# Optimization experiments

Hardware: AMD Instinct MI355X
Metric: run time of the kernel (lower is better)

## Reference

```python
import jax, jax.numpy as jnp
import numpy as np

N_NODES = 20000
N_EDGES = 640000
F_IN = 128
HID = 128


def setup_inputs() -> dict:
    key = jax.random.key(0)
    ks = jax.random.split(key, 12)
    d = {}
    d["x"] = jax.random.normal(ks[0], (N_NODES, F_IN), dtype=jnp.float32)
    d["edge_index"] = jax.random.randint(ks[1], (2, N_EDGES), 0, N_NODES, dtype=jnp.int64)
    d["edge_weight"] = jax.random.uniform(ks[2], (N_EDGES,), dtype=jnp.float32)
    d["h"] = jax.random.normal(ks[3], (N_NODES, HID), dtype=jnp.float32)
    s1 = 1.0 / np.sqrt(F_IN)
    s2 = 1.0 / np.sqrt(HID)
    s3 = 1.0 / np.sqrt(2 * HID)
    d["W1"] = jax.random.uniform(ks[4], (F_IN, HID), jnp.float32, -s1, s1)
    d["b1"] = jnp.zeros((HID,), jnp.float32)
    d["W2"] = jax.random.uniform(ks[5], (HID, HID), jnp.float32, -s2, s2)
    d["b2"] = jnp.zeros((HID,), jnp.float32)
    d["Wu"] = jax.random.uniform(ks[6], (2 * HID, HID), jnp.float32, -s3, s3)
    d["bu"] = jax.random.uniform(ks[7], (HID,), jnp.float32, -s3, s3)
    d["Wr"] = jax.random.uniform(ks[8], (2 * HID, HID), jnp.float32, -s3, s3)
    d["br"] = jax.random.uniform(ks[9], (HID,), jnp.float32, -s3, s3)
    d["Wc"] = jax.random.uniform(ks[10], (2 * HID, HID), jnp.float32, -s3, s3)
    d["bc"] = jax.random.uniform(ks[11], (HID,), jnp.float32, -s3, s3)
    return d


def _gcn_layer(x, W, b, src, dst, norm, n):
    # GCNConv: transform then normalized scatter-add aggregation
    xw = x @ W                                    # [N, out]
    agg = jax.ops.segment_sum(xw[src] * norm[:, None], dst, num_segments=n)
    return agg + b


def reference(x, edge_index, edge_weight, h, W1, b1, W2, b2, Wu, bu, Wr, br, Wc, bc):
    n = x.shape[0]
    loops = jnp.arange(n, dtype=edge_index.dtype)
    src = jnp.concatenate([edge_index[0], loops])
    dst = jnp.concatenate([edge_index[1], loops])
    ew = jnp.concatenate([edge_weight, jnp.ones((n,), edge_weight.dtype)])
    # symmetric GCN normalization with self-loops
    deg = jax.ops.segment_sum(ew, dst, num_segments=n)
    dinv = jnp.where(deg > 0, jax.lax.rsqrt(deg), 0.0)
    norm = dinv[src] * ew * dinv[dst]             # [E+N]
    # 2-layer GCN: in->hid (ReLU) -> hid->hid
    h1 = jax.nn.relu(_gcn_layer(x, W1, b1, src, dst, norm, n))
    g = _gcn_layer(h1, W2, b2, src, dst, norm, n)
    xg = jax.nn.sigmoid(g)                        # [N, HID]
    # GRU-style gating
    xh = jnp.concatenate([xg, h], axis=-1)        # [N, 2*HID]
    u = jax.nn.sigmoid(xh @ Wu + bu)
    r = jax.nn.sigmoid(xh @ Wr + br)
    c = jnp.tanh(jnp.concatenate([xg, r * h], axis=-1) @ Wc + bc)
    return u * h + (1.0 - u) * c
```

## Files before the change

kernel.cpp:

```cpp
#include <hip/hip_runtime.h>
#include <math.h>

#define N_NODES 20000
#define N_EDGES 640000
#define HID 128
#define NPAD 20224
#define NBLK 79
#define NSHARD 8

typedef __attribute__((ext_vector_type(8))) short bf16x8;
typedef __attribute__((ext_vector_type(4))) float f32x4;

#define FIX_SCALE 274877906944.0
#define FIX_MASK ((1ull << 48) - 1)

__device__ inline short f2bf(float f) {
    unsigned u = __builtin_bit_cast(unsigned, f);
    u += 0x7fffu + ((u >> 16) & 1u);
    return (short)(u >> 16);
}
__device__ inline float bf2f(short s) {
    unsigned u = ((unsigned)(unsigned short)s) << 16;
    return __builtin_bit_cast(float, u);
}
__device__ inline float4 unpack_bf4(uint2 v) {
    float4 f;
    f.x = __builtin_bit_cast(float, v.x << 16);
    f.y = __builtin_bit_cast(float, v.x & 0xffff0000u);
    f.z = __builtin_bit_cast(float, v.y << 16);
    f.w = __builtin_bit_cast(float, v.y & 0xffff0000u);
    return f;
}
__device__ inline uint2 pack_bf4(float4 f) {
    uint2 v;
    v.x = (unsigned)(unsigned short)f2bf(f.x) | ((unsigned)(unsigned short)f2bf(f.y) << 16);
    v.y = (unsigned)(unsigned short)f2bf(f.z) | ((unsigned)(unsigned short)f2bf(f.w) << 16);
    return v;
}
__device__ inline bf16x8 cvt8(float4 a0, float4 a1) {
    bf16x8 v;
    v[0] = f2bf(a0.x); v[1] = f2bf(a0.y); v[2] = f2bf(a0.z); v[3] = f2bf(a0.w);
    v[4] = f2bf(a1.x); v[5] = f2bf(a1.y); v[6] = f2bf(a1.z); v[7] = f2bf(a1.w);
    return v;
}

__global__ __launch_bounds__(256) void k_init(unsigned long long* packed) {
    int i = blockIdx.x * 256 + threadIdx.x;
    if (i < NSHARD * NPAD) packed[i] = 0ull;
}

__global__ __launch_bounds__(256) void k_hist(unsigned long long* packed, int* __restrict__ rank,
                                              const int* __restrict__ dst,
                                              const float* __restrict__ ew) {
    int e = blockIdx.x * 256 + threadIdx.x;
    int shard = blockIdx.x & (NSHARD - 1);
    if (e < N_EDGES) {
        int d = dst[e];
        unsigned long long add = (1ull << 48) | (unsigned long long)((double)ew[e] * FIX_SCALE);
        unsigned long long old = atomicAdd(&packed[shard * NPAD + d], add);
        rank[e] = (int)(old >> 48);
    }
}

__global__ __launch_bounds__(256) void k_scan_part(const unsigned long long* __restrict__ packed,
                                                   int* __restrict__ tot, int* __restrict__ bsum) {
    __shared__ int red[256];
    int tid = threadIdx.x;
    int i = blockIdx.x * 256 + tid;
    int t = 0;
    if (i < N_NODES) {
#pragma unroll
        for (int s = 0; s < NSHARD; s++) t += (int)(packed[s * NPAD + i] >> 48);
        tot[i] = t;
    }
    red[tid] = t;
    __syncthreads();
    for (int off = 128; off > 0; off >>= 1) {
        if (tid < off) red[tid] += red[tid + off];
        __syncthreads();
    }
    if (tid == 0) bsum[blockIdx.x] = red[0];
}

__global__ __launch_bounds__(256) void k_scan_final(const unsigned long long* __restrict__ packed,
                                                    const int* __restrict__ tot,
                                                    const int* __restrict__ bsum,
                                                    int* __restrict__ rp, int* __restrict__ sb,
                                                    float* __restrict__ dinv) {
    __shared__ int smem[256];
    __shared__ int red[256];
    int tid = threadIdx.x;
    red[tid] = (tid < blockIdx.x) ? bsum[tid] : 0;
    int i = blockIdx.x * 256 + tid;
    int t = (i < N_NODES) ? tot[i] : 0;
    smem[tid] = t;
    __syncthreads();
    for (int off = 128; off > 0; off >>= 1) {
        if (tid < off) red[tid] += red[tid + off];
        __syncthreads();
    }
    for (int off = 1; off < 256; off <<= 1) {
        int x = (tid >= off) ? smem[tid - off] : 0;
        __syncthreads();
        smem[tid] += x;
        __syncthreads();
    }
    if (i < N_NODES) {
        int excl = smem[tid] - t + red[0];
        rp[i] = excl;
        if (i == N_NODES - 1) rp[N_NODES] = excl + t;
        int acc = excl;
        double deg = 1.0;
#pragma unroll
        for (int s = 0; s < NSHARD; s++) {
            unsigned long long p = packed[s * NPAD + i];
            sb[s * NPAD + i] = acc;
            acc += (int)(p >> 48);
            deg += (double)(p & FIX_MASK) * (1.0 / FIX_SCALE);
        }
        dinv[i] = rsqrtf((float)deg);
    }
}

__global__ __launch_bounds__(256) void k_fill(const int* __restrict__ src,
                                              const int* __restrict__ dst,
                                              const float* __restrict__ ew,
                                              const float* __restrict__ dinv,
                                              const int* __restrict__ sb,
                                              const int* __restrict__ rank,
                                              int2* __restrict__ csr) {
    int e = blockIdx.x * 256 + threadIdx.x;
    int shard = blockIdx.x & (NSHARD - 1);
    if (e < N_EDGES) {
        int s = src[e], d = dst[e];
        int slot = sb[shard * NPAD + d] + rank[e];
        float w = dinv[s] * ew[e] * dinv[d];
        csr[slot] = make_int2(s, __builtin_bit_cast(int, w));
    }
}

__global__ __launch_bounds__(256) void k_wcvt(const float* __restrict__ W1, const float* __restrict__ W2,
                                              const float* __restrict__ Wu, const float* __restrict__ Wr,
                                              const float* __restrict__ Wc,
                                              short* WT1, short* WT2, short* WTu, short* WTr, short* WTc) {
    int i = blockIdx.x * 256 + threadIdx.x;
    if (i < 32768) {
        const float* W = (i < 16384) ? W1 : W2;
        short* T = (i < 16384) ? WT1 : WT2;
        int j = i & 16383;
        int n = j >> 7, k = j & 127;
        T[n * 128 + k] = f2bf(W[k * 128 + n]);
    } else {
        int j = i - 32768;
        const float* W = Wu; short* T = WTu;
        if (j >= 65536)      { W = Wc; T = WTc; j -= 65536; }
        else if (j >= 32768) { W = Wr; T = WTr; j -= 32768; }
        int n = j >> 8, k = j & 255;
        T[n * 256 + k] = f2bf(W[k * 128 + n]);
    }
}

__global__ __launch_bounds__(256) void k_gemm_mfma(const float* __restrict__ Af,
                                                   const short* __restrict__ Ab,
                                                   const short* __restrict__ WT,
                                                   short* __restrict__ Cb) {
    __shared__ short As[16 * 136];
    int tid = threadIdx.x;
    int r0 = blockIdx.x * 16;
    {
        int row = tid >> 4;
        int col0 = (tid & 15) * 8;
        bf16x8 v;
        if (Af) {
            const float* p = Af + (size_t)(r0 + row) * HID + col0;
            v = cvt8(*(const float4*)p, *(const float4*)(p + 4));
        } else {
            v = *(const bf16x8*)(Ab + (size_t)(r0 + row) * HID + col0);
        }
        *(bf16x8*)(&As[row * 136 + col0]) = v;
    }
    __syncthreads();
    int wave = tid >> 6, lane = tid & 63;
    int m = lane & 15, quad = lane >> 4;
    f32x4 acc[2];
    acc[0] = (f32x4){0.f, 0.f, 0.f, 0.f};
    acc[1] = acc[0];
#pragma unroll
    for (int ks = 0; ks < 4; ks++) {
        int k0 = ks * 32 + quad * 8;
        bf16x8 a = *(const bf16x8*)(&As[m * 136 + k0]);
#pragma unroll
        for (int j = 0; j < 2; j++) {
            int n = (wave * 2 + j) * 16 + m;
            bf16x8 b = *(const bf16x8*)(WT + n * 128 + k0);
            acc[j] = __builtin_amdgcn_mfma_f32_16x16x32_bf16(a, b, acc[j], 0, 0, 0);
        }
    }
#pragma unroll
    for (int j = 0; j < 2; j++) {
        int col = (wave * 2 + j) * 16 + m;
#pragma unroll
        for (int rg = 0; rg < 4; rg++) {
            int grow = r0 + quad * 4 + rg;
            Cb[(size_t)grow * HID + col] = f2bf(acc[j][rg]);
        }
    }
}

__global__ __launch_bounds__(256) void k_aggregate(const short* __restrict__ xw,
                                                   short* __restrict__ outb,
                                                   const int* __restrict__ rp,
                                                   const int2* __restrict__ csr,
                                                   const float* __restrict__ dinv,
                                                   const float* __restrict__ bias,
                                                   int act) {
    int node = blockIdx.x * 4 + (threadIdx.x >> 6);
    int lane = threadIdx.x & 63;
    int half = lane >> 5;
    int l = lane & 31;
    float4 acc = {0.f, 0.f, 0.f, 0.f};
    if (half == 0) {
        float dv = dinv[node];
        float dv2 = dv * dv;
        float4 v = unpack_bf4(((const uint2*)(xw + (size_t)node * HID))[l]);
        acc.x = v.x * dv2; acc.y = v.y * dv2; acc.z = v.z * dv2; acc.w = v.w * dv2;
    }
    int j = rp[node], end = rp[node + 1];
    for (; j + 15 < end; j += 16) {
        int2 e[8];
#pragma unroll
        for (int i = 0; i < 8; i++) e[i] = csr[j + 2 * i + half];
        float4 v[8];
#pragma unroll
        for (int i = 0; i < 8; i++) v[i] = unpack_bf4(((const uint2*)(xw + (size_t)e[i].x * HID))[l]);
#pragma unroll
        for (int i = 0; i < 8; i++) {
            float w = __builtin_bit_cast(float, e[i].y);
            acc.x += v[i].x * w; acc.y += v[i].y * w; acc.z += v[i].z * w; acc.w += v[i].w * w;
        }
    }
    for (; j + 7 < end; j += 8) {
        int2 e[4];
#pragma unroll
        for (int i = 0; i < 4; i++) e[i] = csr[j + 2 * i + half];
        float4 v[4];
#pragma unroll
        for (int i = 0; i < 4; i++) v[i] = unpack_bf4(((const uint2*)(xw + (size_t)e[i].x * HID))[l]);
#pragma unroll
        for (int i = 0; i < 4; i++) {
            float w = __builtin_bit_cast(float, e[i].y);
            acc.x += v[i].x * w; acc.y += v[i].y * w; acc.z += v[i].z * w; acc.w += v[i].w * w;
        }
    }
    for (; j + 1 < end; j += 2) {
        int2 e0 = csr[j + half];
        float4 v0 = unpack_bf4(((const uint2*)(xw + (size_t)e0.x * HID))[l]);
        float w0 = __builtin_bit_cast(float, e0.y);
        acc.x += v0.x * w0; acc.y += v0.y * w0; acc.z += v0.z * w0; acc.w += v0.w * w0;
    }
    if (j < end && half == 0) {
        int2 e0 = csr[j];
        float4 v0 = unpack_bf4(((const uint2*)(xw + (size_t)e0.x * HID))[l]);
        float w0 = __builtin_bit_cast(float, e0.y);
        acc.x += v0.x * w0; acc.y += v0.y * w0; acc.z += v0.z * w0; acc.w += v0.w * w0;
    }
    acc.x += __shfl_xor(acc.x, 32);
    acc.y += __shfl_xor(acc.y, 32);
    acc.z += __shfl_xor(acc.z, 32);
    acc.w += __shfl_xor(acc.w, 32);
    if (half == 0) {
        float4 b = ((const float4*)bias)[l];
        acc.x += b.x; acc.y += b.y; acc.z += b.z; acc.w += b.w;
        if (act == 0) {
            acc.x = fmaxf(acc.x, 0.f); acc.y = fmaxf(acc.y, 0.f);
            acc.z = fmaxf(acc.z, 0.f); acc.w = fmaxf(acc.w, 0.f);
        } else {
            acc.x = 1.f / (1.f + __expf(-acc.x)); acc.y = 1.f / (1.f + __expf(-acc.y));
            acc.z = 1.f / (1.f + __expf(-acc.z)); acc.w = 1.f / (1.f + __expf(-acc.w));
        }
        ((uint2*)(outb + (size_t)node * HID))[l] = pack_bf4(acc);
    }
}

__global__ __launch_bounds__(256) void k_gate(const short* __restrict__ xgb,
                                              const float* __restrict__ hf,
                                              const short* __restrict__ WTu, const short* __restrict__ WTr,
                                              const short* __restrict__ WTc,
                                              const float* __restrict__ pbu, const float* __restrict__ pbr,
                                              const float* __restrict__ pbc,
                                              float* __restrict__ out) {
    __shared__ short Xs[16 * 264];
    int tid = threadIdx.x;
    int r0 = blockIdx.x * 16;
#pragma unroll
    for (int i = 0; i < 2; i++) {
        int c = tid + i * 256;
        int row = c >> 5;
        int col0 = (c & 31) * 8;
        int grow = r0 + row;
        bf16x8 v;
        if (col0 < 128) {
            v = *(const bf16x8*)(xgb + (size_t)grow * HID + col0);
        } else {
            const float* p = hf + (size_t)grow * HID + (col0 - 128);
            v = cvt8(*(const float4*)p, *(const float4*)(p + 4));
        }
        *(bf16x8*)(&Xs[row * 264 + col0]) = v;
    }
    __syncthreads();
    int wave = tid >> 6, lane = tid & 63;
    int m = lane & 15, quad = lane >> 4;
    f32x4 au[2], ar[2];
    au[0] = (f32x4){0.f, 0.f, 0.f, 0.f};
    au[1] = au[0]; ar[0] = au[0]; ar[1] = au[0];
#pragma unroll
    for (int ks = 0; ks < 8; ks++) {
        int k0 = ks * 32 + quad * 8;
        bf16x8 a = *(const bf16x8*)(&Xs[m * 264 + k0]);
#pragma unroll
        for (int j = 0; j < 2; j++) {
            int n = (wave * 2 + j) * 16 + m;
            bf16x8 bu_f = *(const bf16x8*)(WTu + n * 256 + k0);
            au[j] = __builtin_amdgcn_mfma_f32_16x16x32_bf16(a, bu_f, au[j], 0, 0, 0);
            bf16x8 br_f = *(const bf16x8*)(WTr + n * 256 + k0);
            ar[j] = __builtin_amdgcn_mfma_f32_16x16x32_bf16(a, br_f, ar[j], 0, 0, 0);
        }
    }
    __syncthreads();
#pragma unroll
    for (int j = 0; j < 2; j++) {
        int col = (wave * 2 + j) * 16 + m;
        float brv = pbr[col];
#pragma unroll
        for (int rg = 0; rg < 4; rg++) {
            int trow = quad * 4 + rg;
            float rv = 1.f / (1.f + __expf(-(ar[j][rg] + brv)));
            float hv = bf2f(Xs[trow * 264 + 128 + col]);
            Xs[trow * 264 + 128 + col] = f2bf(rv * hv);
        }
    }
    __syncthreads();
    f32x4 ac[2];
    ac[0] = (f32x4){0.f, 0.f, 0.f, 0.f};
    ac[1] = ac[0];
#pragma unroll
    for (int ks = 0; ks < 8; ks++) {
        int k0 = ks * 32 + quad * 8;
        bf16x8 a = *(const bf16x8*)(&Xs[m * 264 + k0]);
#pragma unroll
        for (int j = 0; j < 2; j++) {
            int n = (wave * 2 + j) * 16 + m;
            bf16x8 bc_f = *(const bf16x8*)(WTc + n * 256 + k0);
            ac[j] = __builtin_amdgcn_mfma_f32_16x16x32_bf16(a, bc_f, ac[j], 0, 0, 0);
        }
    }
#pragma unroll
    for (int j = 0; j < 2; j++) {
        int col = (wave * 2 + j) * 16 + m;
        float buv = pbu[col], bcv = pbc[col];
#pragma unroll
        for (int rg = 0; rg < 4; rg++) {
            int grow = r0 + quad * 4 + rg;
            float uv = 1.f / (1.f + __expf(-(au[j][rg] + buv)));
            float cv = tanhf(ac[j][rg] + bcv);
            float hv = hf[(size_t)grow * HID + col];
            out[(size_t)grow * HID + col] = uv * hv + (1.f - uv) * cv;
        }
    }
}

extern "C" void kernel_launch(void* const* d_in, const int* in_sizes, int n_in,
                              void* d_out, int out_size, void* d_ws, size_t ws_size,
                              hipStream_t stream) {
    const float* x  = (const float*)d_in[0];
    const int*   ei = (const int*)d_in[1];
    const float* ew = (const float*)d_in[2];
    const float* h  = (const float*)d_in[3];
    const float* W1 = (const float*)d_in[4];
    const float* b1 = (const float*)d_in[5];
    const float* W2 = (const float*)d_in[6];
    const float* b2 = (const float*)d_in[7];
    const float* Wu = (const float*)d_in[8];
    const float* bu = (const float*)d_in[9];
    const float* Wr = (const float*)d_in[10];
    const float* br = (const float*)d_in[11];
    const float* Wc = (const float*)d_in[12];
    const float* bc = (const float*)d_in[13];
    const int* src = ei;
    const int* dst = ei + N_EDGES;
    float* out = (float*)d_out;

    const size_t NH = (size_t)N_NODES * HID;
    float* ws = (float*)d_ws;
    float* dinv = ws;
    int*   rp   = (int*)(ws + NPAD);
    unsigned long long* packed = (unsigned long long*)(ws + 2 * NPAD);
    int*   sb   = (int*)(ws + 18 * NPAD);
    int*   tot  = (int*)(ws + 26 * NPAD);
    int*   bsum = (int*)(ws + 27 * NPAD);
    int*   rank = (int*)(ws + 27 * NPAD + 128);
    int2*  csr  = (int2*)(ws + 27 * NPAD + 128 + N_EDGES);
    short* xw  = (short*)(ws + 27 * NPAD + 128 + 3 * N_EDGES);
    short* h1b = xw + NH;
    short* xgb = h1b + NH;
    short* WT1 = xgb + NH;
    short* WT2 = WT1 + 16384;
    short* WTu = WT2 + 16384;
    short* WTr = WTu + 32768;
    short* WTc = WTr + 32768;

    k_init<<<(NSHARD * NPAD + 255) / 256, 256, 0, stream>>>(packed);
    k_hist<<<N_EDGES / 256, 256, 0, stream>>>(packed, rank, dst, ew);
    k_scan_part<<<NBLK, 256, 0, stream>>>(packed, tot, bsum);
    k_scan_final<<<NBLK, 256, 0, stream>>>(packed, tot, bsum, rp, sb, dinv);
    k_fill<<<N_EDGES / 256, 256, 0, stream>>>(src, dst, ew, dinv, sb, rank, csr);

    k_wcvt<<<512, 256, 0, stream>>>(W1, W2, Wu, Wr, Wc, WT1, WT2, WTu, WTr, WTc);

    k_gemm_mfma<<<N_NODES / 16, 256, 0, stream>>>(x, nullptr, WT1, xw);
    k_aggregate<<<N_NODES / 4, 256, 0, stream>>>(xw, h1b, rp, csr, dinv, b1, 0);
    k_gemm_mfma<<<N_NODES / 16, 256, 0, stream>>>(nullptr, h1b, WT2, xw);
    k_aggregate<<<N_NODES / 4, 256, 0, stream>>>(xw, xgb, rp, csr, dinv, b2, 1);
    k_gate<<<N_NODES / 16, 256, 0, stream>>>(xgb, h, WTu, WTr, WTc, bu, br, bc, out);
}
```

Measured before the change: 252.1 us.

## Fuse GCN aggregation with following GEMMs and merge setup kernels

Merges the weight conversion with the histogram-buffer zeroing, and runs the edge histogram alongside the first-layer GEMM in a single launch. Each aggregation now writes its result straight into shared memory, where the next GEMM (W2, or the gating GEMMs) consumes it. This removes launches and the round-trips of the h1 and xg intermediates through global memory. The cost is that aggregation is now done by 16-row blocks, with each wave handling 4 nodes in sequence, which gives less parallelism and may leave blocks imbalanced by node degree.

```diff
diff --git a/kernel.cpp b/kernel.cpp
--- a/kernel.cpp
+++ b/kernel.cpp
@@ -44,21 +44,142 @@
     return v;
 }
 
-__global__ __launch_bounds__(256) void k_init(unsigned long long* packed) {
-    int i = blockIdx.x * 256 + threadIdx.x;
-    if (i < NSHARD * NPAD) packed[i] = 0ull;
-}
-
-__global__ __launch_bounds__(256) void k_hist(unsigned long long* packed, int* __restrict__ rank,
-                                              const int* __restrict__ dst,
-                                              const float* __restrict__ ew) {
-    int e = blockIdx.x * 256 + threadIdx.x;
-    int shard = blockIdx.x & (NSHARD - 1);
-    if (e < N_EDGES) {
+__device__ inline float4 agg_node(int node, int half, int l,
+                                  const short* __restrict__ xw,
+                                  const int* __restrict__ rp,
+                                  const int2* __restrict__ csr,
+                                  const float* __restrict__ dinv) {
+    float4 acc = {0.f, 0.f, 0.f, 0.f};
+    if (half == 0) {
+        float dv = dinv[node];
+        float dv2 = dv * dv;
+        float4 v = unpack_bf4(((const uint2*)(xw + (size_t)node * HID))[l]);
+        acc.x = v.x * dv2; acc.y = v.y * dv2; acc.z = v.z * dv2; acc.w = v.w * dv2;
+    }
+    int j = rp[node], end = rp[node + 1];
+    for (; j + 15 < end; j += 16) {
+        int2 e[8];
+#pragma unroll
+        for (int i = 0; i < 8; i++) e[i] = csr[j + 2 * i + half];
+        float4 v[8];
+#pragma unroll
+        for (int i = 0; i < 8; i++) v[i] = unpack_bf4(((const uint2*)(xw + (size_t)e[i].x * HID))[l]);
+#pragma unroll
+        for (int i = 0; i < 8; i++) {
+            float w = __builtin_bit_cast(float, e[i].y);
+            acc.x += v[i].x * w; acc.y += v[i].y * w; acc.z += v[i].z * w; acc.w += v[i].w * w;
+        }
+    }
+    for (; j + 7 < end; j += 8) {
+        int2 e[4];
+#pragma unroll
+        for (int i = 0; i < 4; i++) e[i] = csr[j + 2 * i + half];
+        float4 v[4];
+#pragma unroll
+        for (int i = 0; i < 4; i++) v[i] = unpack_bf4(((const uint2*)(xw + (size_t)e[i].x * HID))[l]);
+#pragma unroll
+        for (int i = 0; i < 4; i++) {
+            float w = __builtin_bit_cast(float, e[i].y);
+            acc.x += v[i].x * w; acc.y += v[i].y * w; acc.z += v[i].z * w; acc.w += v[i].w * w;
+        }
+    }
+    for (; j + 1 < end; j += 2) {
+        int2 e0 = csr[j + half];
+        float4 v0 = unpack_bf4(((const uint2*)(xw + (size_t)e0.x * HID))[l]);
+        float w0 = __builtin_bit_cast(float, e0.y);
+        acc.x += v0.x * w0; acc.y += v0.y * w0; acc.z += v0.z * w0; acc.w += v0.w * w0;
+    }
+    if (j < end && half == 0) {
+        int2 e0 = csr[j];
+        float4 v0 = unpack_bf4(((const uint2*)(xw + (size_t)e0.x * HID))[l]);
+        float w0 = __builtin_bit_cast(float, e0.y);
+        acc.x += v0.x * w0; acc.y += v0.y * w0; acc.z += v0.z * w0; acc.w += v0.w * w0;
+    }
+    acc.x += __shfl_xor(acc.x, 32);
+    acc.y += __shfl_xor(acc.y, 32);
+    acc.z += __shfl_xor(acc.z, 32);
+    acc.w += __shfl_xor(acc.w, 32);
+    return acc;
+}
+
+__global__ __launch_bounds__(256) void k_prep(const float* __restrict__ W1, const float* __restrict__ W2,
+                                              const float* __restrict__ Wu, const float* __restrict__ Wr,
+                                              const float* __restrict__ Wc,
+                                              short* WT1, short* WT2, short* WTu, short* WTr, short* WTc,
+                                              unsigned long long* packed) {
+    int b = blockIdx.x;
+    int tid = threadIdx.x;
+    if (b < 512) {
+        int i = b * 256 + tid;
+        if (i < 32768) {
+            const float* W = (i < 16384) ? W1 : W2;
+            short* T = (i < 16384) ? WT1 : WT2;
+            int j = i & 16383;
+            int n = j >> 7, k = j & 127;
+            T[n * 128 + k] = f2bf(W[k * 128 + n]);
+        } else {
+            int j = i - 32768;
+            const float* W = Wu; short* T = WTu;
+            if (j >= 65536)      { W = Wc; T = WTc; j -= 65536; }
+            else if (j >= 32768) { W = Wr; T = WTr; j -= 32768; }
+            int n = j >> 8, k = j & 255;
+            T[n * 256 + k] = f2bf(W[k * 128 + n]);
+        }
+    } else {
+        int i = (b - 512) * 256 + tid;
+        if (i < NSHARD * NPAD) packed[i] = 0ull;
+    }
+}
+
+__global__ __launch_bounds__(256) void k_hist_gemm(unsigned long long* packed, int* __restrict__ rank,
+                                                   const int* __restrict__ dst,
+                                                   const float* __restrict__ ew,
+                                                   const float* __restrict__ x,
+                                                   const short* __restrict__ WT1,
+                                                   short* __restrict__ xw) {
+    __shared__ short As[16 * 136];
+    int tid = threadIdx.x;
+    if (blockIdx.x < 2500) {
+        int e = blockIdx.x * 256 + tid;
+        int shard = blockIdx.x & (NSHARD - 1);
         int d = dst[e];
         unsigned long long add = (1ull << 48) | (unsigned long long)((double)ew[e] * FIX_SCALE);
         unsigned long long old = atomicAdd(&packed[shard * NPAD + d], add);
         rank[e] = (int)(old >> 48);
+        return;
+    }
+    int r0 = (blockIdx.x - 2500) * 16;
+    {
+        int row = tid >> 4;
+        int col0 = (tid & 15) * 8;
+        const float* p = x + (size_t)(r0 + row) * HID + col0;
+        *(bf16x8*)(&As[row * 136 + col0]) = cvt8(*(const float4*)p, *(const float4*)(p + 4));
+    }
+    __syncthreads();
+    int wave = tid >> 6, lane = tid & 63;
+    int m = lane & 15, quad = lane >> 4;
+    f32x4 acc[2];
+    acc[0] = (f32x4){0.f, 0.f, 0.f, 0.f};
+    acc[1] = acc[0];
+#pragma unroll
+    for (int ks = 0; ks < 4; ks++) {
+        int k0 = ks * 32 + quad * 8;
+        bf16x8 a = *(const bf16x8*)(&As[m * 136 + k0]);
+#pragma unroll
+        for (int j = 0; j < 2; j++) {
+            int n = (wave * 2 + j) * 16 + m;
+            bf16x8 b = *(const bf16x8*)(WT1 + n * 128 + k0);
+            acc[j] = __builtin_amdgcn_mfma_f32_16x16x32_bf16(a, b, acc[j], 0, 0, 0);
+        }
+    }
+#pragma unroll
+    for (int j = 0; j < 2; j++) {
+        int col = (wave * 2 + j) * 16 + m;
+#pragma unroll
+        for (int rg = 0; rg < 4; rg++) {
+            int grow = r0 + quad * 4 + rg;
+            xw[(size_t)grow * HID + col] = f2bf(acc[j][rg]);
+        }
     }
 }
 
@@ -139,176 +260,92 @@
     }
 }
 
-__global__ __launch_bounds__(256) void k_wcvt(const float* __restrict__ W1, const float* __restrict__ W2,
-                                              const float* __restrict__ Wu, const float* __restrict__ Wr,
-                                              const float* __restrict__ Wc,
-                                              short* WT1, short* WT2, short* WTu, short* WTr, short* WTc) {
-    int i = blockIdx.x * 256 + threadIdx.x;
-    if (i < 32768) {
-        const float* W = (i < 16384) ? W1 : W2;
-        short* T = (i < 16384) ? WT1 : WT2;
-        int j = i & 16383;
-        int n = j >> 7, k = j & 127;
-        T[n * 128 + k] = f2bf(W[k * 128 + n]);
-    } else {
-        int j = i - 32768;
-        const float* W = Wu; short* T = WTu;
-        if (j >= 65536)      { W = Wc; T = WTc; j -= 65536; }
-        else if (j >= 32768) { W = Wr; T = WTr; j -= 32768; }
-        int n = j >> 8, k = j & 255;
-        T[n * 256 + k] = f2bf(W[k * 128 + n]);
-    }
-}
-
-__global__ __launch_bounds__(256) void k_gemm_mfma(const float* __restrict__ Af,
-                                                   const short* __restrict__ Ab,
-                                                   const short* __restrict__ WT,
-                                                   short* __restrict__ Cb) {
+__global__ __launch_bounds__(256) void k_agg_gemm(const short* __restrict__ xw,
+                                                  const int* __restrict__ rp,
+                                                  const int2* __restrict__ csr,
+                                                  const float* __restrict__ dinv,
+                                                  const float* __restrict__ bias,
+                                                  const short* __restrict__ WT2,
+                                                  short* __restrict__ xw2) {
     __shared__ short As[16 * 136];
     int tid = threadIdx.x;
+    int wave = tid >> 6, lane = tid & 63;
+    int half = lane >> 5, l = lane & 31;
+    int r0 = blockIdx.x * 16;
+    float4 b = ((const float4*)bias)[l];
+#pragma unroll
+    for (int w = 0; w < 4; w++) {
+        int trow = wave * 4 + w;
+        float4 acc = agg_node(r0 + trow, half, l, xw, rp, csr, dinv);
+        if (half == 0) {
+            acc.x = fmaxf(acc.x + b.x, 0.f); acc.y = fmaxf(acc.y + b.y, 0.f);
+            acc.z = fmaxf(acc.z + b.z, 0.f); acc.w = fmaxf(acc.w + b.w, 0.f);
+            *(uint2*)(&As[trow * 136 + 4 * l]) = pack_bf4(acc);
+        }
+    }
+    __syncthreads();
+    int m = lane & 15, quad = lane >> 4;
+    f32x4 acc[2];
+    acc[0] = (f32x4){0.f, 0.f, 0.f, 0.f};
+    acc[1] = acc[0];
+#pragma unroll
+    for (int ks = 0; ks < 4; ks++) {
+        int k0 = ks * 32 + quad * 8;
+        bf16x8 a = *(const bf16x8*)(&As[m * 136 + k0]);
+#pragma unroll
+        for (int j = 0; j < 2; j++) {
+            int n = (wave * 2 + j) * 16 + m;
+            bf16x8 bw = *(const bf16x8*)(WT2 + n * 128 + k0);
+            acc[j] = __builtin_amdgcn_mfma_f32_16x16x32_bf16(a, bw, acc[j], 0, 0, 0);
+        }
+    }
+#pragma unroll
+    for (int j = 0; j < 2; j++) {
+        int col = (wave * 2 + j) * 16 + m;
+#pragma unroll
+        for (int rg = 0; rg < 4; rg++) {
+            int grow = r0 + quad * 4 + rg;
+            xw2[(size_t)grow * HID + col] = f2bf(acc[j][rg]);
+        }
+    }
+}
+
+__global__ __launch_bounds__(256) void k_agg_gate(const short* __restrict__ xw2,
+                                                  const int* __restrict__ rp,
+                                                  const int2* __restrict__ csr,
+                                                  const float* __restrict__ dinv,
+                                                  const float* __restrict__ bias2,
+                                                  const float* __restrict__ hf,
+                                                  const short* __restrict__ WTu, const short* __restrict__ WTr,
+                                                  const short* __restrict__ WTc,
+                                                  const float* __restrict__ pbu, const float* __restrict__ pbr,
+                                                  const float* __restrict__ pbc,
+                                                  float* __restrict__ out) {
+    __shared__ short Xs[16 * 264];
+    int tid = threadIdx.x;
+    int wave = tid >> 6, lane = tid & 63;
+    int half = lane >> 5, l = lane & 31;
     int r0 = blockIdx.x * 16;
     {
         int row = tid >> 4;
         int col0 = (tid & 15) * 8;
-        bf16x8 v;
-        if (Af) {
-            const float* p = Af + (size_t)(r0 + row) * HID + col0;
-            v = cvt8(*(const float4*)p, *(const float4*)(p + 4));
-        } else {
-            v = *(const bf16x8*)(Ab + (size_t)(r0 + row) * HID + col0);
-        }
-        *(bf16x8*)(&As[row * 136 + col0]) = v;
-    }
-    __syncthreads();
-    int wave = tid >> 6, lane = tid & 63;
-    int m = lane & 15, quad = lane >> 4;
-    f32x4 acc[2];
-    acc[0] = (f32x4){0.f, 0.f, 0.f, 0.f};
-    acc[1] = acc[0];
-#pragma unroll
-    for (int ks = 0; ks < 4; ks++) {
-        int k0 = ks * 32 + quad * 8;
-        bf16x8 a = *(const bf16x8*)(&As[m * 136 + k0]);
-#pragma unroll
-        for (int j = 0; j < 2; j++) {
-            int n = (wave * 2 + j) * 16 + m;
-            bf16x8 b = *(const bf16x8*)(WT + n * 128 + k0);
-            acc[j] = __builtin_amdgcn_mfma_f32_16x16x32_bf16(a, b, acc[j], 0, 0, 0);
-        }
-    }
-#pragma unroll
-    for (int j = 0; j < 2; j++) {
-        int col = (wave * 2 + j) * 16 + m;
-#pragma unroll
-        for (int rg = 0; rg < 4; rg++) {
-            int grow = r0 + quad * 4 + rg;
-            Cb[(size_t)grow * HID + col] = f2bf(acc[j][rg]);
-        }
-    }
-}
-
-__global__ __launch_bounds__(256) void k_aggregate(const short* __restrict__ xw,
-                                                   short* __restrict__ outb,
-                                                   const int* __restrict__ rp,
-                                                   const int2* __restrict__ csr,
-                                                   const float* __restrict__ dinv,
-                                                   const float* __restrict__ bias,
-                                                   int act) {
-    int node = blockIdx.x * 4 + (threadIdx.x >> 6);
-    int lane = threadIdx.x & 63;
-    int half = lane >> 5;
-    int l = lane & 31;
-    float4 acc = {0.f, 0.f, 0.f, 0.f};
-    if (half == 0) {
-        float dv = dinv[node];
-        float dv2 = dv * dv;
-        float4 v = unpack_bf4(((const uint2*)(xw + (size_t)node * HID))[l]);
-        acc.x = v.x * dv2; acc.y = v.y * dv2; acc.z = v.z * dv2; acc.w = v.w * dv2;
-    }
-    int j = rp[node], end = rp[node + 1];
-    for (; j + 15 < end; j += 16) {
-        int2 e[8];
-#pragma unroll
-        for (int i = 0; i < 8; i++) e[i] = csr[j + 2 * i + half];
-        float4 v[8];
-#pragma unroll
-        for (int i = 0; i < 8; i++) v[i] = unpack_bf4(((const uint2*)(xw + (size_t)e[i].x * HID))[l]);
-#pragma unroll
-        for (int i = 0; i < 8; i++) {
-            float w = __builtin_bit_cast(float, e[i].y);
-            acc.x += v[i].x * w; acc.y += v[i].y * w; acc.z += v[i].z * w; acc.w += v[i].w * w;
-        }
-    }
-    for (; j + 7 < end; j += 8) {
-        int2 e[4];
-#pragma unroll
-        for (int i = 0; i < 4; i++) e[i] = csr[j + 2 * i + half];
-        float4 v[4];
-#pragma unroll
-        for (int i = 0; i < 4; i++) v[i] = unpack_bf4(((const uint2*)(xw + (size_t)e[i].x * HID))[l]);
-#pragma unroll
-        for (int i = 0; i < 4; i++) {
-            float w = __builtin_bit_cast(float, e[i].y);
-            acc.x += v[i].x * w; acc.y += v[i].y * w; acc.z += v[i].z * w; acc.w += v[i].w * w;
-        }
-    }
-    for (; j + 1 < end; j += 2) {
-        int2 e0 = csr[j + half];
-        float4 v0 = unpack_bf4(((const uint2*)(xw + (size_t)e0.x * HID))[l]);
-        float w0 = __builtin_bit_cast(float, e0.y);
-        acc.x += v0.x * w0; acc.y += v0.y * w0; acc.z += v0.z * w0; acc.w += v0.w * w0;
-    }
-    if (j < end && half == 0) {
-        int2 e0 = csr[j];
-        float4 v0 = unpack_bf4(((const uint2*)(xw + (size_t)e0.x * HID))[l]);
-        float w0 = __builtin_bit_cast(float, e0.y);
-        acc.x += v0.x * w0; acc.y += v0.y * w0; acc.z += v0.z * w0; acc.w += v0.w * w0;
-    }
-    acc.x += __shfl_xor(acc.x, 32);
-    acc.y += __shfl_xor(acc.y, 32);
-    acc.z += __shfl_xor(acc.z, 32);
-    acc.w += __shfl_xor(acc.w, 32);
-    if (half == 0) {
-        float4 b = ((const float4*)bias)[l];
-        acc.x += b.x; acc.y += b.y; acc.z += b.z; acc.w += b.w;
-        if (act == 0) {
-            acc.x = fmaxf(acc.x, 0.f); acc.y = fmaxf(acc.y, 0.f);
-            acc.z = fmaxf(acc.z, 0.f); acc.w = fmaxf(acc.w, 0.f);
-        } else {
-            acc.x = 1.f / (1.f + __expf(-acc.x)); acc.y = 1.f / (1.f + __expf(-acc.y));
-            acc.z = 1.f / (1.f + __expf(-acc.z)); acc.w = 1.f / (1.f + __expf(-acc.w));
-        }
-        ((uint2*)(outb + (size_t)node * HID))[l] = pack_bf4(acc);
-    }
-}
-
-__global__ __launch_bounds__(256) void k_gate(const short* __restrict__ xgb,
-                                              const float* __restrict__ hf,
-                                              const short* __restrict__ WTu, const short* __restrict__ WTr,
-                                              const short* __restrict__ WTc,
-                                              const float* __restrict__ pbu, const float* __restrict__ pbr,
-                                              const float* __restrict__ pbc,
-                                              float* __restrict__ out) {
-    __shared__ short Xs[16 * 264];
-    int tid = threadIdx.x;
-    int r0 = blockIdx.x * 16;
-#pragma unroll
-    for (int i = 0; i < 2; i++) {
-        int c = tid + i * 256;
-        int row = c >> 5;
-        int col0 = (c & 31) * 8;
-        int grow = r0 + row;
-        bf16x8 v;
-        if (col0 < 128) {
-            v = *(const bf16x8*)(xgb + (size_t)grow * HID + col0);
-        } else {
-            const float* p = hf + (size_t)grow * HID + (col0 - 128);
-            v = cvt8(*(const float4*)p, *(const float4*)(p + 4));
-        }
-        *(bf16x8*)(&Xs[row * 264 + col0]) = v;
-    }
-    __syncthreads();
-    int wave = tid >> 6, lane = tid & 63;
+        const float* p = hf + (size_t)(r0 + row) * HID + col0;
+        *(bf16x8*)(&Xs[row * 264 + 128 + col0]) = cvt8(*(const float4*)p, *(const float4*)(p + 4));
+    }
+    float4 b2 = ((const float4*)bias2)[l];
+#pragma unroll
+    for (int w = 0; w < 4; w++) {
+        int trow = wave * 4 + w;
+        float4 acc = agg_node(r0 + trow, half, l, xw2, rp, csr, dinv);
+        if (half == 0) {
+            acc.x = 1.f / (1.f + __expf(-(acc.x + b2.x)));
+            acc.y = 1.f / (1.f + __expf(-(acc.y + b2.y)));
+            acc.z = 1.f / (1.f + __expf(-(acc.z + b2.z)));
+            acc.w = 1.f / (1.f + __expf(-(acc.w + b2.w)));
+            *(uint2*)(&Xs[trow * 264 + 4 * l]) = pack_bf4(acc);
+        }
+    }
+    __syncthreads();
     int m = lane & 15, quad = lane >> 4;
     f32x4 au[2], ar[2];
     au[0] = (f32x4){0.f, 0.f, 0.f, 0.f};
@@ -400,26 +437,21 @@
     int*   bsum = (int*)(ws + 27 * NPAD);
     int*   rank = (int*)(ws + 27 * NPAD + 128);
     int2*  csr  = (int2*)(ws + 27 * NPAD + 128 + N_EDGES);
-    short* xw  = (short*)(ws + 27 * NPAD + 128 + 3 * N_EDGES);
-    short* h1b = xw + NH;
-    short* xgb = h1b + NH;
-    short* WT1 = xgb + NH;
+    short* xw   = (short*)(ws + 27 * NPAD + 128 + 3 * N_EDGES);
+    short* xw2  = xw + NH;
+    short* WT1 = xw2 + NH;
     short* WT2 = WT1 + 16384;
     short* WTu = WT2 + 16384;
     short* WTr = WTu + 32768;
     short* WTc = WTr + 32768;
 
-    k_init<<<(NSHARD * NPAD + 255) / 256, 256, 0, stream>>>(packed);
-    k_hist<<<N_EDGES / 256, 256, 0, stream>>>(packed, rank, dst, ew);
+    k_prep<<<512 + (NSHARD * NPAD + 255) / 256, 256, 0, stream>>>(
+        W1, W2, Wu, Wr, Wc, WT1, WT2, WTu, WTr, WTc, packed);
+    k_hist_gemm<<<2500 + N_NODES / 16, 256, 0, stream>>>(packed, rank, dst, ew, x, WT1, xw);
     k_scan_part<<<NBLK, 256, 0, stream>>>(packed, tot, bsum);
     k_scan_final<<<NBLK, 256, 0, stream>>>(packed, tot, bsum, rp, sb, dinv);
     k_fill<<<N_EDGES / 256, 256, 0, stream>>>(src, dst, ew, dinv, sb, rank, csr);
-
-    k_wcvt<<<512, 256, 0, stream>>>(W1, W2, Wu, Wr, Wc, WT1, WT2, WTu, WTr, WTc);
-
-    k_gemm_mfma<<<N_NODES / 16, 256, 0, stream>>>(x, nullptr, WT1, xw);
-    k_aggregate<<<N_NODES / 4, 256, 0, stream>>>(xw, h1b, rp, csr, dinv, b1, 0);
-    k_gemm_mfma<<<N_NODES / 16, 256, 0, stream>>>(nullptr, h1b, WT2, xw);
-    k_aggregate<<<N_NODES / 4, 256, 0, stream>>>(xw, xgb, rp, csr, dinv, b2, 1);
-    k_gate<<<N_NODES / 16, 256, 0, stream>>>(xgb, h, WTu, WTr, WTc, bu, br, bc, out);
-}
+    k_agg_gemm<<<N_NODES / 16, 256, 0, stream>>>(xw, rp, csr, dinv, b1, WT2, xw2);
+    k_agg_gate<<<N_NODES / 16, 256, 0, stream>>>(xw2, rp, csr, dinv, b2, h,
+                                                 WTu, WTr, WTc, bu, br, bc, out);
+}
```

After: 255.4 us. About the same (+1.3%).
